# Kernel tuning notes

Hardware: AMD Instinct MI355X
Metric: run time of the kernel (lower is better)

## Reference

```python
import jax, jax.numpy as jnp
import numpy as np

Q_DIM = 768
KV_DIM = 1024
NUM_HEADS = 12
HEAD_DIM = Q_DIM // NUM_HEADS  # 64


def setup_inputs() -> dict:
    key = jax.random.key(0)
    ks = jax.random.split(key, 10)
    B, N_q, N_kv = 16, 64, 4096
    s_q = 1.0 / np.sqrt(Q_DIM)
    s_kv = 1.0 / np.sqrt(KV_DIM)
    return {
        "query": jax.random.normal(ks[0], (B, N_q, Q_DIM), dtype=jnp.float32),
        "kv": jax.random.normal(ks[1], (B, N_kv, KV_DIM), dtype=jnp.float32),
        "Wq": jax.random.normal(ks[2], (Q_DIM, Q_DIM), dtype=jnp.float32) * s_q,
        "bq": jnp.zeros((Q_DIM,), dtype=jnp.float32),
        "Wk": jax.random.normal(ks[3], (KV_DIM, Q_DIM), dtype=jnp.float32) * s_kv,
        "bk": jnp.zeros((Q_DIM,), dtype=jnp.float32),
        "Wv": jax.random.normal(ks[4], (KV_DIM, Q_DIM), dtype=jnp.float32) * s_kv,
        "bv": jnp.zeros((Q_DIM,), dtype=jnp.float32),
        "Wo": jax.random.normal(ks[5], (Q_DIM, Q_DIM), dtype=jnp.float32) * s_q,
        "bo": jnp.zeros((Q_DIM,), dtype=jnp.float32),
    }


def reference(query, kv, Wq, bq, Wk, bk, Wv, bv, Wo, bo):
    B, N_q, C = query.shape
    N_kv = kv.shape[1]
    H, D = NUM_HEADS, HEAD_DIM
    scale = D ** -0.5
    # projections -> (B, H, N, D)
    q = (query @ Wq + bq).reshape(B, N_q, H, D).transpose(0, 2, 1, 3)
    k = (kv @ Wk + bk).reshape(B, N_kv, H, D).transpose(0, 2, 1, 3)
    v = (kv @ Wv + bv).reshape(B, N_kv, H, D).transpose(0, 2, 1, 3)
    # scores (B, H, N_q, N_kv) -- explicitly materialized as in the original
    attn = jnp.einsum("bhqd,bhkd->bhqk", q, k) * scale
    attn = jax.nn.softmax(attn, axis=-1)
    x = jnp.einsum("bhqk,bhkd->bhqd", attn, v)
    x = x.transpose(0, 2, 1, 3).reshape(B, N_q, C)
    return x @ Wo + bo
```

## Files before the change

kernel.cpp:

```cpp
#include <hip/hip_runtime.h>
#include <hip/hip_bf16.h>

typedef unsigned short u16;
typedef unsigned int u32;
typedef short v8s __attribute__((ext_vector_type(8)));
typedef float v4f __attribute__((ext_vector_type(4)));

#define NB 16
#define NQ 64
#define NKV 4096
#define QD 768
#define KD 1024
#define NH 12
#define HD 64

__device__ __forceinline__ u16 f2bf(float f) {
  union { float f; u32 u; } c; c.f = f;
  u32 u = c.u;
  u += 0x7FFFu + ((u >> 16) & 1u);
  return (u16)(u >> 16);
}
__device__ __forceinline__ u32 pack2(float a, float b) {
  return (u32)f2bf(a) | ((u32)f2bf(b) << 16);
}

__device__ __forceinline__ void async16(const void* g, void* l) {
  __builtin_amdgcn_global_load_lds(
      (const __attribute__((address_space(1))) void*)g,
      (__attribute__((address_space(3))) void*)l, 16, 0, 0);
}

__global__ __launch_bounds__(256) void prep_wT_dual(
    const float* __restrict__ W0, const float* __restrict__ W1,
    u16* __restrict__ T0, u16* __restrict__ T1, int K, int N) {
  __shared__ float tile[32][33];
  const float* W = blockIdx.z ? W1 : W0;
  u16* WT = blockIdx.z ? T1 : T0;
  const int n0 = blockIdx.x * 32, k0 = blockIdx.y * 32;
  const int tr = threadIdx.x >> 5, tc = threadIdx.x & 31;
#pragma unroll
  for (int r = tr; r < 32; r += 8) tile[r][tc] = W[(size_t)(k0 + r) * N + n0 + tc];
  __syncthreads();
#pragma unroll
  for (int r = tr; r < 32; r += 8) WT[(size_t)(n0 + r) * K + k0 + tc] = f2bf(tile[tc][r]);
}

__global__ __launch_bounds__(256) void conv8(const float* __restrict__ s,
                                             u16* __restrict__ d, int n8) {
  int i = blockIdx.x * 256 + threadIdx.x;
  if (i >= n8) return;
  const float4* sp = (const float4*)s + (size_t)i * 2;
  float4 a = sp[0], b = sp[1];
  uint4 o;
  o.x = pack2(a.x, a.y); o.y = pack2(a.z, a.w);
  o.z = pack2(b.x, b.y); o.w = pack2(b.z, b.w);
  ((uint4*)d)[i] = o;
}

__global__ void concat_bias(const float* __restrict__ a, const float* __restrict__ b,
                            float* __restrict__ o) {
  int i = blockIdx.x * 256 + threadIdx.x;
  if (i < 768) o[i] = a[i];
  else if (i < 1536) o[i] = b[i - 768];
}

template<bool OUT_BF16, bool KV_SPLIT>
__global__ __launch_bounds__(256) void gemm_a(
    const u16* __restrict__ A, const u16* __restrict__ BT,
    const float* __restrict__ bias, void* __restrict__ Cp, u16* __restrict__ Vtp,
    int M, int N, int K)
{
  __shared__ __align__(16) u16 As[128][32];
  __shared__ __align__(16) u16 Bs[128][32];
  const int bn0 = blockIdx.x * 128, bm0 = blockIdx.y * 128;
  const int t = threadIdx.x, lane = t & 63, wv = t >> 6;
  const int wm = (wv & 1) * 64, wn = (wv >> 1) * 64;
  const int lm = lane & 15, quad = lane >> 4;
  const int srow = lane >> 2;
  const int sc = (((lane & 3) ^ ((srow >> 1) & 3)) * 8);

  const int r0 = wv * 32, r1 = wv * 32 + 16;
  const u16* aP0 = A  + (size_t)(bm0 + r0 + srow) * K + sc;
  const u16* aP1 = A  + (size_t)(bm0 + r1 + srow) * K + sc;
  const u16* bP0 = BT + (size_t)(bn0 + r0 + srow) * K + sc;
  const u16* bP1 = BT + (size_t)(bn0 + r1 + srow) * K + sc;

  const int swz = (lm >> 1) & 3;

  v4f acc[4][4];
  v4f zero = {0.f, 0.f, 0.f, 0.f};
#pragma unroll
  for (int i = 0; i < 4; ++i)
#pragma unroll
    for (int j = 0; j < 4; ++j) acc[i][j] = zero;

  for (int k0 = 0; k0 < K; k0 += 32) {
    async16(aP0, &As[r0][0]);
    async16(aP1, &As[r1][0]);
    async16(bP0, &Bs[r0][0]);
    async16(bP1, &Bs[r1][0]);
    aP0 += 32; aP1 += 32; bP0 += 32; bP1 += 32;
    __builtin_amdgcn_s_waitcnt(0);
    __syncthreads();
    v8s a[4], b[4];
#pragma unroll
    for (int mt = 0; mt < 4; ++mt)
      a[mt] = *(const v8s*)&As[wm + mt * 16 + lm][(quad ^ swz) * 8];
#pragma unroll
    for (int nt = 0; nt < 4; ++nt)
      b[nt] = *(const v8s*)&Bs[wn + nt * 16 + lm][(quad ^ swz) * 8];
#pragma unroll
    for (int mt = 0; mt < 4; ++mt)
#pragma unroll
      for (int nt = 0; nt < 4; ++nt)
        acc[mt][nt] = __builtin_amdgcn_mfma_f32_16x16x32_bf16(a[mt], b[nt], acc[mt][nt], 0, 0, 0);
    __syncthreads();
  }

  if constexpr (KV_SPLIT) {
    if (bn0 < 768) {
      u16* kp_ = (u16*)Cp;
#pragma unroll
      for (int mt = 0; mt < 4; ++mt)
#pragma unroll
        for (int nt = 0; nt < 4; ++nt) {
          int col = bn0 + wn + nt * 16 + lm;
          float bs = bias[col];
#pragma unroll
          for (int r = 0; r < 4; ++r) {
            int grow = bm0 + wm + mt * 16 + quad * 4 + r;
            kp_[(size_t)grow * 768 + col] = f2bf(acc[mt][nt][r] + bs);
          }
        }
    } else {
#pragma unroll
      for (int mt = 0; mt < 4; ++mt)
#pragma unroll
        for (int nt = 0; nt < 4; ++nt) {
          int col = bn0 + wn + nt * 16 + lm;
          int cv = col - 768;
          float bs = bias[col];
          int grow0 = bm0 + wm + mt * 16 + quad * 4;
          int b_ = grow0 >> 12, kvr = grow0 & 4095;
          uint2 o;
          o.x = pack2(acc[mt][nt][0] + bs, acc[mt][nt][1] + bs);
          o.y = pack2(acc[mt][nt][2] + bs, acc[mt][nt][3] + bs);
          *(uint2*)&Vtp[((size_t)(b_ * 768 + cv)) * 4096 + kvr] = o;
        }
    }
  } else {
#pragma unroll
    for (int mt = 0; mt < 4; ++mt)
#pragma unroll
      for (int nt = 0; nt < 4; ++nt)
#pragma unroll
        for (int r = 0; r < 4; ++r) {
          int row = bm0 + wm + mt * 16 + quad * 4 + r;
          int col = bn0 + wn + nt * 16 + lm;
          float v = acc[mt][nt][r] + bias[col];
          if constexpr (OUT_BF16) ((u16*)Cp)[(size_t)row * N + col] = f2bf(v);
          else                    ((float*)Cp)[(size_t)row * N + col] = v;
        }
  }
}

__global__ __launch_bounds__(256) void attn_k(
    const u16* __restrict__ qp,
    const u16* __restrict__ kp,
    const u16* __restrict__ vT,
    u16* __restrict__ xo)
{
  __shared__ __align__(16) u16 Ps[4][16][40];
  __shared__ float Mw[4][16], Lw[4][16];
  __shared__ float Os[4][16][64];
  const int lane = threadIdx.x & 63, w = threadIdx.x >> 6;
  const int lm = lane & 15, quad = lane >> 4;
  const int blk = blockIdx.x, slab = blk & 3, bh = blk >> 2;
  const int b = bh / NH, h = bh - b * NH;
  const int qr0 = b * NQ + slab * 16;

  const u16* qptr = qp + (size_t)(qr0 + lm) * QD + h * HD + quad * 8;
  v8s aq0 = *(const v8s*)qptr;
  v8s aq1 = *(const v8s*)(qptr + 32);

  const u16* kb = kp + (size_t)b * NKV * QD + h * HD;
  const u16* vb = vT + (size_t)(b * QD + h * HD) * NKV;

  float mst[4], lst[4];
  v4f O[4];
  v4f zero = {0.f, 0.f, 0.f, 0.f};
#pragma unroll
  for (int r = 0; r < 4; ++r) { mst[r] = -INFINITY; lst[r] = 0.f; }
#pragma unroll
  for (int d = 0; d < 4; ++d) O[d] = zero;

  const float scale = 0.125f;

  v8s kf[2][4], vf[2][4];
  auto loadchunk = [&](int j0, int bi) {
    const u16* k0p = kb + (size_t)(j0 + lm) * QD + quad * 8;
    const u16* k1p = kb + (size_t)(j0 + 16 + lm) * QD + quad * 8;
    kf[bi][0] = *(const v8s*)k0p;
    kf[bi][1] = *(const v8s*)(k0p + 32);
    kf[bi][2] = *(const v8s*)k1p;
    kf[bi][3] = *(const v8s*)(k1p + 32);
#pragma unroll
    for (int d = 0; d < 4; ++d)
      vf[bi][d] = *(const v8s*)&vb[(size_t)(d * 16 + lm) * NKV + j0 + quad * 8];
  };
  auto compute = [&](int bi) {
    v4f S0 = zero, S1 = zero;
    S0 = __builtin_amdgcn_mfma_f32_16x16x32_bf16(aq0, kf[bi][0], S0, 0, 0, 0);
    S0 = __builtin_amdgcn_mfma_f32_16x16x32_bf16(aq1, kf[bi][1], S0, 0, 0, 0);
    S1 = __builtin_amdgcn_mfma_f32_16x16x32_bf16(aq0, kf[bi][2], S1, 0, 0, 0);
    S1 = __builtin_amdgcn_mfma_f32_16x16x32_bf16(aq1, kf[bi][3], S1, 0, 0, 0);

    float p0[4], p1[4], rmax[4];
#pragma unroll
    for (int r = 0; r < 4; ++r) {
      p0[r] = S0[r] * scale; p1[r] = S1[r] * scale;
      rmax[r] = fmaxf(p0[r], p1[r]);
    }
#pragma unroll
    for (int off = 1; off <= 8; off <<= 1)
#pragma unroll
      for (int r = 0; r < 4; ++r) rmax[r] = fmaxf(rmax[r], __shfl_xor(rmax[r], off, 64));

    float alpha[4], rsum[4];
#pragma unroll
    for (int r = 0; r < 4; ++r) {
      float mn = fmaxf(mst[r], rmax[r]);
      alpha[r] = __expf(mst[r] - mn);
      p0[r] = __expf(p0[r] - mn);
      p1[r] = __expf(p1[r] - mn);
      mst[r] = mn;
      rsum[r] = p0[r] + p1[r];
    }
#pragma unroll
    for (int off = 1; off <= 8; off <<= 1)
#pragma unroll
      for (int r = 0; r < 4; ++r) rsum[r] += __shfl_xor(rsum[r], off, 64);
#pragma unroll
    for (int r = 0; r < 4; ++r) {
      lst[r] = lst[r] * alpha[r] + rsum[r];
      Ps[w][quad * 4 + r][lm] = f2bf(p0[r]);
      Ps[w][quad * 4 + r][16 + lm] = f2bf(p1[r]);
    }
#pragma unroll
    for (int d = 0; d < 4; ++d)
#pragma unroll
      for (int r = 0; r < 4; ++r) O[d][r] *= alpha[r];
    v8s aP = *(const v8s*)&Ps[w][lm][quad * 8];
#pragma unroll
    for (int d = 0; d < 4; ++d)
      O[d] = __builtin_amdgcn_mfma_f32_16x16x32_bf16(aP, vf[bi][d], O[d], 0, 0, 0);
  };

  const int base = w * 1024;
  loadchunk(base, 0);
  for (int j0 = base; j0 < base + 1024; j0 += 64) {
    loadchunk(j0 + 32, 1);
    compute(0);
    if (j0 + 64 < base + 1024) loadchunk(j0 + 64, 0);
    compute(1);
  }

  if (lm == 0) {
#pragma unroll
    for (int r = 0; r < 4; ++r) {
      Mw[w][quad * 4 + r] = mst[r];
      Lw[w][quad * 4 + r] = lst[r];
    }
  }
  __syncthreads();
#pragma unroll
  for (int r = 0; r < 4; ++r) {
    int row = quad * 4 + r;
    float M = fmaxf(fmaxf(Mw[0][row], Mw[1][row]), fmaxf(Mw[2][row], Mw[3][row]));
    float sc = __expf(mst[r] - M);
#pragma unroll
    for (int d = 0; d < 4; ++d) Os[w][row][d * 16 + lm] = O[d][r] * sc;
  }
  __syncthreads();
#pragma unroll
  for (int i = 0; i < 4; ++i) {
    int row = w * 4 + i;
    float M = fmaxf(fmaxf(Mw[0][row], Mw[1][row]), fmaxf(Mw[2][row], Mw[3][row]));
    float L = Lw[0][row] * __expf(Mw[0][row] - M) + Lw[1][row] * __expf(Mw[1][row] - M)
            + Lw[2][row] * __expf(Mw[2][row] - M) + Lw[3][row] * __expf(Mw[3][row] - M);
    float o = Os[0][row][lane] + Os[1][row][lane] + Os[2][row][lane] + Os[3][row][lane];
    xo[(size_t)(qr0 + row) * QD + h * HD + lane] = f2bf(o / L);
  }
}

extern "C" void kernel_launch(void* const* d_in, const int* in_sizes, int n_in,
                              void* d_out, int out_size, void* d_ws, size_t ws_size,
                              hipStream_t stream) {
  const float* query = (const float*)d_in[0];
  const float* kv    = (const float*)d_in[1];
  const float* Wq    = (const float*)d_in[2];
  const float* bq    = (const float*)d_in[3];
  const float* Wk    = (const float*)d_in[4];
  const float* bk    = (const float*)d_in[5];
  const float* Wv    = (const float*)d_in[6];
  const float* bv    = (const float*)d_in[7];
  const float* Wo    = (const float*)d_in[8];
  const float* bo    = (const float*)d_in[9];
  float* out = (float*)d_out;
  char* ws = (char*)d_ws;

  u16*   WkvT = (u16*)(ws);
  float* bkv  = (float*)(ws + 3145728);
  u16*   WqT  = (u16*)(ws + 3151872);
  u16*   WoT  = (u16*)(ws + 4331520);
  u16*   qbf  = (u16*)(ws + 5511168);
  u16*   qp   = (u16*)(ws + 7084032);
  u16*   xov  = (u16*)(ws + 8656896);
  u16*   kp   = (u16*)(ws + 10229760);
  u16*   vT   = (u16*)(ws + 110893056);
  u16*   kvbf = (u16*)(ws + 211556352);

  prep_wT_dual<<<dim3(24, 32, 2), 256, 0, stream>>>(Wk, Wv, WkvT, WkvT + 768 * 1024, KD, QD);
  prep_wT_dual<<<dim3(24, 24, 2), 256, 0, stream>>>(Wq, Wo, WqT, WoT, QD, QD);
  concat_bias<<<6, 256, 0, stream>>>(bk, bv, bkv);
  conv8<<<32768, 256, 0, stream>>>(kv, kvbf, NB * NKV * KD / 8);
  gemm_a<true, true><<<dim3(12, 512), 256, 0, stream>>>(kvbf, WkvT, bkv, kp, vT,
                                                        65536, 1536, KD);
  conv8<<<384, 256, 0, stream>>>(query, qbf, NB * NQ * QD / 8);
  gemm_a<true, false><<<dim3(6, 8), 256, 0, stream>>>(qbf, WqT, bq, qp, nullptr,
                                                      1024, QD, QD);
  attn_k<<<NB * NH * 4, 256, 0, stream>>>(qp, kp, vT, xov);
  gemm_a<false, false><<<dim3(6, 8), 256, 0, stream>>>(xov, WoT, bo, out, nullptr,
                                                       1024, QD, QD);
}
```

Baseline: 953.3 us.

## Add dedicated 256x256-tile KV projection GEMM with double-buffered async LDS loads

Replaces the generic gemm_a used for the large K/V projection (65536x1536x1024) with a specialised kernel. It uses 256x256 output tiles, 512 threads, double-buffered LDS filled by async global-to-LDS copies, and an XOR-swizzled layout. A grouped block-ID swizzle improves L2 reuse, and s_setprio raises priority around the MFMA bursts. The goal is more reuse per loaded byte and overlap of loads with MFMA work on the dominant GEMM, at the cost of higher LDS and register pressure, which may lower occupancy.

```diff
diff --git a/kernel.cpp b/kernel.cpp
--- a/kernel.cpp
+++ b/kernel.cpp
@@ -161,6 +161,133 @@
           if constexpr (OUT_BF16) ((u16*)Cp)[(size_t)row * N + col] = f2bf(v);
           else                    ((float*)Cp)[(size_t)row * N + col] = v;
         }
+  }
+}
+
+#define KVK 1024
+#define KVKT 16
+#define SLOT 32768
+
+__global__ __launch_bounds__(512, 2) void gemm_kv256(
+    const u16* __restrict__ A, const u16* __restrict__ BT,
+    const float* __restrict__ bias,
+    u16* __restrict__ kp_, u16* __restrict__ vT_)
+{
+  __shared__ __align__(16) u16 As[2][256][64];
+  __shared__ __align__(16) u16 Bs[2][256][64];
+
+  const int bid = blockIdx.x;
+  const int swzb = (bid & 7) * 192 + (bid >> 3);
+  const int tn = swzb % 6, tm = swzb / 6;
+  const int bn0 = tn * 256, bm0 = tm * 256;
+
+  const int tid = threadIdx.x;
+  const int lane = tid & 63, wv = tid >> 6;
+  const int lm = lane & 15, quad = lane >> 4;
+  const int wrow = wv >> 2, wcol = wv & 3;
+
+  const int srow = tid >> 3;
+  const int schunk = (tid & 7) ^ (srow & 7);
+  const u16* aS = A  + (size_t)(bm0 + srow) * KVK + schunk * 8;
+  const u16* bS = BT + (size_t)(bn0 + srow) * KVK + schunk * 8;
+  char* const aD = (char*)&As[0][0][0] + wv * 1024;
+  char* const bD = (char*)&Bs[0][0][0] + wv * 1024;
+
+  const int c0 = (quad ^ (lm & 7)) * 16;
+  const int c1 = ((quad + 4) ^ (lm & 7)) * 16;
+  const char* const aR = (const char*)&As[0][0][0] + (wrow * 128 + lm) * 128;
+  const char* const bR = (const char*)&Bs[0][0][0] + (wcol * 64 + lm) * 128;
+
+  v4f acc[8][4];
+  v4f zero = {0.f, 0.f, 0.f, 0.f};
+#pragma unroll
+  for (int i = 0; i < 8; ++i)
+#pragma unroll
+    for (int j = 0; j < 4; ++j) acc[i][j] = zero;
+
+#pragma unroll
+  for (int r = 0; r < 4; ++r) {
+    async16(aS + (size_t)r * (64 * KVK), aD + r * 8192);
+    async16(bS + (size_t)r * (64 * KVK), bD + r * 8192);
+  }
+  aS += 64; bS += 64;
+  __syncthreads();
+
+  int soff = 0;
+#pragma unroll 1
+  for (int t = 0; t < KVKT; ++t) {
+    const int noff = soff ^ SLOT;
+    if (t + 1 < KVKT) {
+#pragma unroll
+      for (int r = 0; r < 4; ++r) {
+        async16(aS + (size_t)r * (64 * KVK), aD + noff + r * 8192);
+        async16(bS + (size_t)r * (64 * KVK), bD + noff + r * 8192);
+      }
+      aS += 64; bS += 64;
+    }
+    v8s bf[4][2];
+#pragma unroll
+    for (int nt = 0; nt < 4; ++nt) {
+      const char* bp = bR + soff + nt * 2048;
+      bf[nt][0] = *(const v8s*)(bp + c0);
+      bf[nt][1] = *(const v8s*)(bp + c1);
+    }
+#pragma unroll
+    for (int p = 0; p < 4; ++p) {
+      v8s af[2][2];
+#pragma unroll
+      for (int i = 0; i < 2; ++i) {
+        const char* ap = aR + soff + (p * 2 + i) * 2048;
+        af[i][0] = *(const v8s*)(ap + c0);
+        af[i][1] = *(const v8s*)(ap + c1);
+      }
+      __builtin_amdgcn_s_barrier();
+      asm volatile("s_waitcnt lgkmcnt(0)" ::: "memory");
+      __builtin_amdgcn_sched_barrier(0);
+      __builtin_amdgcn_s_setprio(1);
+#pragma unroll
+      for (int i = 0; i < 2; ++i)
+#pragma unroll
+        for (int nt = 0; nt < 4; ++nt) {
+          acc[p * 2 + i][nt] = __builtin_amdgcn_mfma_f32_16x16x32_bf16(
+              af[i][0], bf[nt][0], acc[p * 2 + i][nt], 0, 0, 0);
+          acc[p * 2 + i][nt] = __builtin_amdgcn_mfma_f32_16x16x32_bf16(
+              af[i][1], bf[nt][1], acc[p * 2 + i][nt], 0, 0, 0);
+        }
+      __builtin_amdgcn_s_setprio(0);
+      __builtin_amdgcn_s_barrier();
+    }
+    __syncthreads();
+    soff = noff;
+  }
+
+  if (bn0 < 768) {
+#pragma unroll
+    for (int mt = 0; mt < 8; ++mt)
+#pragma unroll
+      for (int nt = 0; nt < 4; ++nt) {
+        const int col = bn0 + wcol * 64 + nt * 16 + lm;
+        const float bs = bias[col];
+        const int grow0 = bm0 + wrow * 128 + mt * 16 + quad * 4;
+#pragma unroll
+        for (int r = 0; r < 4; ++r)
+          kp_[(size_t)(grow0 + r) * 768 + col] = f2bf(acc[mt][nt][r] + bs);
+      }
+  } else {
+#pragma unroll
+    for (int mt = 0; mt < 8; ++mt)
+#pragma unroll
+      for (int nt = 0; nt < 4; ++nt) {
+        const int col = bn0 + wcol * 64 + nt * 16 + lm;
+        const int cv = col - 768;
+        const float bs = bias[col];
+        const int grow0 = bm0 + wrow * 128 + mt * 16 + quad * 4;
+        const int b_ = grow0 >> 12, kvr = grow0 & 4095;
+        uint2 o;
+        o.x = pack2(acc[mt][nt][0] + bs, acc[mt][nt][1] + bs);
+        o.y = pack2(acc[mt][nt][2] + bs, acc[mt][nt][3] + bs);
+        *(uint2*)&vT_[((size_t)(b_ * 768 + cv)) * 4096 + kvr] = o;
+      }
   }
 }
 
@@ -324,8 +451,7 @@
   prep_wT_dual<<<dim3(24, 24, 2), 256, 0, stream>>>(Wq, Wo, WqT, WoT, QD, QD);
   concat_bias<<<6, 256, 0, stream>>>(bk, bv, bkv);
   conv8<<<32768, 256, 0, stream>>>(kv, kvbf, NB * NKV * KD / 8);
-  gemm_a<true, true><<<dim3(12, 512), 256, 0, stream>>>(kvbf, WkvT, bkv, kp, vT,
-                                                        65536, 1536, KD);
+  gemm_kv256<<<1536, 512, 0, stream>>>(kvbf, WkvT, bkv, kp, vT);
   conv8<<<384, 256, 0, stream>>>(query, qbf, NB * NQ * QD / 8);
   gemm_a<true, false><<<dim3(6, 8), 256, 0, stream>>>(qbf, WqT, bq, qp, nullptr,
                                                       1024, QD, QD);
```

Result: faster. 897.6 us (-5.8%).
